# Kernel tuning notes

Measured on AMD Instinct MI355X. Metric: run time of the kernel, lower is better.

The kernel has to match this reference:

```python
import jax, jax.numpy as jnp
import numpy as np

H = 512          # hidden_dim
T = 80           # future_length
M = 6            # num_modes
OD = 2           # output_dim
B = 2048         # batch
TEMP = 1.2


def _lin_params(key, out_dim, in_dim, scale=0.02):
    kw, kb = jax.random.split(key)
    W = jax.random.normal(kw, (out_dim, in_dim), jnp.float32) * scale
    b = jax.random.normal(kb, (out_dim,), jnp.float32) * scale
    return W, b


def _per_mode(key, out_dim, in_dim, scale=0.02):
    ks = jax.random.split(key, M)
    Ws, bs = [], []
    for k in ks:
        W, b = _lin_params(k, out_dim, in_dim, scale)
        Ws.append(W); bs.append(b)
    return jnp.stack(Ws), jnp.stack(bs)


def setup_inputs() -> dict:
    key = jax.random.key(0)
    ks = jax.random.split(key, 20)
    inp = {}
    inp['composed_features'] = jax.random.normal(ks[0], (B, H), jnp.float32)
    # mode_decoders: Linear(H,2H) ReLU [Dropout] Linear(2H,H) ReLU [Dropout] Linear(H,H)
    inp['md_W1'], inp['md_b1'] = _per_mode(ks[1], 2 * H, H)
    inp['md_W2'], inp['md_b2'] = _per_mode(ks[2], H, 2 * H)
    inp['md_W3'], inp['md_b3'] = _per_mode(ks[3], H, H)
    # initial_hidden_projections: Linear(H, 2H)
    inp['ih_W'], inp['ih_b'] = _per_mode(ks[4], 2 * H, H)
    # time_projection (shared): Linear(1, H//2) ReLU Linear(H//2, H)
    inp['tp_W1'], inp['tp_b1'] = _lin_params(ks[5], H // 2, 1)
    inp['tp_W2'], inp['tp_b2'] = _lin_params(ks[6], H, H // 2)
    # feedback_projections: Linear(OD, H//2)
    inp['fb_W'], inp['fb_b'] = _per_mode(ks[7], H // 2, OD)
    # LSTM (2 layers, torch gate order i,f,g,o), per mode
    inp['l0_Wih'], inp['l0_bih'] = _per_mode(ks[8], 4 * H, H)
    inp['l0_Whh'], inp['l0_bhh'] = _per_mode(ks[9], 4 * H, H)
    inp['l1_Wih'], inp['l1_bih'] = _per_mode(ks[10], 4 * H, H)
    inp['l1_Whh'], inp['l1_bhh'] = _per_mode(ks[11], 4 * H, H)
    # output_projections: Linear(H,H) ReLU [Dropout] Linear(H,OD)
    inp['op_W1'], inp['op_b1'] = _per_mode(ks[12], H, H)
    inp['op_W2'], inp['op_b2'] = _per_mode(ks[13], OD, H)
    # confidence_head (shared): Linear(H, H//2) ReLU [Dropout] Linear(H//2, M)
    inp['cf_W1'], inp['cf_b1'] = _lin_params(ks[14], H // 2, H)
    inp['cf_W2'], inp['cf_b2'] = _lin_params(ks[15], M, H // 2)
    return inp


def _lstm_cell(x, h, c, Wih, Whh, bih, bhh):
    g = x @ Wih.T + h @ Whh.T + (bih + bhh)
    i, f, gg, o = jnp.split(g, 4, axis=-1)
    c_new = jax.nn.sigmoid(f) * c + jax.nn.sigmoid(i) * jnp.tanh(gg)
    h_new = jax.nn.sigmoid(o) * jnp.tanh(c_new)
    return h_new, c_new


def _forward(composed_features,
             md_W1, md_b1, md_W2, md_b2, md_W3, md_b3,
             ih_W, ih_b, tp_W1, tp_b1, tp_W2, tp_b2,
             fb_W, fb_b,
             l0_Wih, l0_bih, l0_Whh, l0_bhh,
             l1_Wih, l1_bih, l1_Whh, l1_bhh,
             op_W1, op_b1, op_W2, op_b2,
             cf_W1, cf_b1, cf_W2, cf_b2):
    x = composed_features
    bsz = x.shape[0]
    # shared time embeddings for all steps: [T, H]
    t_norm = (jnp.arange(T, dtype=jnp.float32) / (T - 1))[:, None]
    time_embs = jax.nn.relu(t_norm @ tp_W1.T + tp_b1) @ tp_W2.T + tp_b2

    def run_mode(mW1, mb1, mW2, mb2, mW3, mb3, iW, ib, fW, fb,
                 W0i, b0i, W0h, b0h, W1i, b1i, W1h, b1h,
                 oW1, ob1, oW2, ob2):
        # mode decoder (dropout = identity in eval)
        mf = jax.nn.relu(x @ mW1.T + mb1)
        mf = jax.nn.relu(mf @ mW2.T + mb2)
        mf = mf @ mW3.T + mb3                      # [B, H]
        init = x @ iW.T + ib                       # [B, 2H]
        h0 = init[:, :H]; c0 = init[:, H:]
        carry = (h0, c0, h0, c0, jnp.zeros((bsz, OD), x.dtype))
        pad = H - H // 2

        def step(carry, te_t):
            h0, c0, h1, c1, prev = carry
            fb_half = prev @ fW.T + fb             # [B, H//2]
            fb_full = jnp.pad(fb_half, ((0, 0), (0, pad)))
            xin = mf + 0.5 * te_t[None, :] + 0.3 * fb_full
            h0, c0 = _lstm_cell(xin, h0, c0, W0i, W0h, b0i, b0h)
            h1, c1 = _lstm_cell(h0, h1, c1, W1i, W1h, b1i, b1h)
            out = jax.nn.relu(h1 @ oW1.T + ob1) @ oW2.T + ob2  # [B, OD]
            return (h0, c0, h1, c1, out), out

        _, outs = jax.lax.scan(step, carry, time_embs)   # [T, B, OD]
        traj = jnp.transpose(outs, (1, 0, 2))            # [B, T, OD]
        return traj.at[:, 0, :].set(0.0)

    trajs = jax.vmap(run_mode)(md_W1, md_b1, md_W2, md_b2, md_W3, md_b3,
                               ih_W, ih_b, fb_W, fb_b,
                               l0_Wih, l0_bih, l0_Whh, l0_bhh,
                               l1_Wih, l1_bih, l1_Whh, l1_bhh,
                               op_W1, op_b1, op_W2, op_b2)  # [M, B, T, OD]
    trajectories = jnp.transpose(trajs, (1, 0, 2, 3))       # [B, M, T, OD]
    logits = jax.nn.relu(x @ cf_W1.T + cf_b1) @ cf_W2.T + cf_b2  # [B, M]
    confidences = jax.nn.softmax(logits / TEMP, axis=-1)
    return trajectories, confidences, logits


def reference(composed_features,
              md_W1, md_b1, md_W2, md_b2, md_W3, md_b3,
              ih_W, ih_b, tp_W1, tp_b1, tp_W2, tp_b2,
              fb_W, fb_b,
              l0_Wih, l0_bih, l0_Whh, l0_bhh,
              l1_Wih, l1_bih, l1_Whh, l1_bhh,
              op_W1, op_b1, op_W2, op_b2,
              cf_W1, cf_b1, cf_W2, cf_b2):
    return _forward(composed_features,
                    md_W1, md_b1, md_W2, md_b2, md_W3, md_b3,
                    ih_W, ih_b, tp_W1, tp_b1, tp_W2, tp_b2,
                    fb_W, fb_b,
                    l0_Wih, l0_bih, l0_Whh, l0_bhh,
                    l1_Wih, l1_bih, l1_Whh, l1_bhh,
                    op_W1, op_b1, op_W2, op_b2,
                    cf_W1, cf_b1, cf_W2, cf_b2)
```

## Files before the change

### kernel.cpp

```cpp
#include <hip/hip_runtime.h>
#include <cstdint>

typedef __bf16 bf16;
typedef __bf16 bf16x8 __attribute__((ext_vector_type(8)));
typedef float f32x4 __attribute__((ext_vector_type(4)));

#define DI __device__ __forceinline__

#define BATCH 2048
#define HD 512
#define NM 6

DI float sigmoidf_(float x){ return 1.0f / (1.0f + __expf(-x)); }
DI float tanhf_(float x){
  float a = __expf(-2.0f * fabsf(x));
  float t = (1.0f - a) / (1.0f + a);
  return __builtin_copysignf(t, x);
}

__global__ void k_diag(float* out, float wsmb){
  if (threadIdx.x == 0 && blockIdx.x == 0) out[0] = wsmb * 1.0e6f;
}

template<bool GATES, bool DUAL>
__global__ void k_pack(bf16* __restrict__ dst, const float* __restrict__ s1,
                       const float* __restrict__ s2, int K, int NROW, int ksplit)
{
  long idx = (long)blockIdx.x * 256 + threadIdx.x;
  int kper = K >> 3;
  int k0 = (int)(idx % kper) * 8;
  long rest = idx / kper;
  int p = (int)(rest % NROW);
  int mm = (int)(rest / NROW);
  int r;
  if (GATES){
    int nb2 = p >> 7, hi = (p >> 6) & 1, g = (p >> 4) & 3, jl = p & 15;
    r = g * 512 + nb2 * 32 + hi * 16 + jl;
  } else r = p;
  const float* src;
  if (DUAL){
    if (k0 >= ksplit) src = s2 + ((long)mm * NROW + r) * ksplit + (k0 - ksplit);
    else              src = s1 + ((long)mm * NROW + r) * ksplit + k0;
  } else {
    src = s1 + ((long)mm * NROW + r) * K + k0;
  }
  f32x4 v0 = *(const f32x4*)(src);
  f32x4 v1 = *(const f32x4*)(src + 4);
  bf16x8 o;
  #pragma unroll
  for (int k = 0; k < 4; ++k){ o[k] = (bf16)v0[k]; o[4+k] = (bf16)v1[k]; }
  *(bf16x8*)(dst + ((long)mm * NROW + p) * K + k0) = o;
}

__global__ void k_temb(bf16* tembb, const float* tpW1, const float* tpb1,
                       const float* tpW2, const float* tpb2)
{
  int t = blockIdx.x; int tid = threadIdx.x;
  __shared__ float rq[256];
  float tn = (t < 80) ? (float)t / 79.0f : 0.0f;
  rq[tid] = fmaxf(tn * tpW1[tid] + tpb1[tid], 0.0f);
  __syncthreads();
  for (int d = tid; d < 512; d += 256){
    float s = tpb2[d];
    const float* w = tpW2 + d * 256;
    for (int q = 0; q < 256; ++q) s += rq[q] * w[q];
    tembb[t * 512 + d] = (bf16)((t < 80) ? 0.5f * s : 0.0f);
  }
}

__global__ void k_biases(float* bias0p, float* bias1p,
                         const float* l0bih, const float* l0bhh,
                         const float* l1bih, const float* l1bhh,
                         const float* l0Wih, const float* fbb)
{
  int idx = blockIdx.x * 256 + threadIdx.x;
  int m = idx >> 11, p = idx & 2047;
  int nb2 = p >> 7, hi = (p >> 6) & 1, g = (p >> 4) & 3, jl = p & 15;
  int r = g * 512 + nb2 * 32 + hi * 16 + jl;
  bias1p[idx] = l1bih[m * 2048 + r] + l1bhh[m * 2048 + r];
  const float* wrow = l0Wih + ((long)m * 2048 + r) * 512;
  const float* fb = fbb + m * 256;
  float acc = 0.0f;
  for (int q = 0; q < 256; ++q) acc += fb[q] * wrow[q];
  bias0p[idx] = l0bih[m * 2048 + r] + l0bhh[m * 2048 + r] + 0.3f * acc;
}

__global__ void k_feffp(float* feffp, const float* fbW, const float* l0Wih)
{
  int idx = blockIdx.x * 256 + threadIdx.x;
  int p = idx & 2047, o = (idx >> 11) & 1, m = idx >> 12;
  int nb2 = p >> 7, hi = (p >> 6) & 1, g = (p >> 4) & 3, jl = p & 15;
  int r = g * 512 + nb2 * 32 + hi * 16 + jl;
  const float* wrow = l0Wih + ((long)m * 2048 + r) * 512;
  float acc = 0.0f;
  for (int q = 0; q < 256; ++q) acc += fbW[((long)m * 256 + q) * 2 + o] * wrow[q];
  feffp[((long)m * 2 + o) * 2048 + p] = 0.3f * acc;
}

__global__ void k_zero(float* part, float* traj)
{
  int i = blockIdx.x * 256 + threadIdx.x;
  part[i] = 0.0f;
  if (i < 24576){
    int od = i & 1, mm = (i >> 1) % 6, b = i / 12;
    traj[b * 960 + mm * 160 + od] = 0.0f;
  }
}

__global__ void k_logits(const bf16* lt1, const float* cfW2, const float* cfb2,
                         float* conf, float* logitsOut)
{
  int b = blockIdx.x * 256 + threadIdx.x;
  float acc[6];
  #pragma unroll
  for (int mm = 0; mm < 6; ++mm) acc[mm] = cfb2[mm];
  for (int q = 0; q < 256; ++q){
    float xv = (float)lt1[b * 256 + q];
    #pragma unroll
    for (int mm = 0; mm < 6; ++mm) acc[mm] += xv * cfW2[mm * 256 + q];
  }
  float mx = acc[0];
  #pragma unroll
  for (int mm = 1; mm < 6; ++mm) mx = fmaxf(mx, acc[mm]);
  float e[6], s = 0.0f;
  #pragma unroll
  for (int mm = 0; mm < 6; ++mm){ e[mm] = __expf((acc[mm] - mx) * (1.0f / 1.2f)); s += e[mm]; }
  float inv = 1.0f / s;
  #pragma unroll
  for (int mm = 0; mm < 6; ++mm){
    logitsOut[b * 6 + mm] = acc[mm];
    conf[b * 6 + mm] = e[mm] * inv;
  }
}

__global__ void k_red(const float* part, const float* opb2, float* traj)
{
  int i = blockIdx.x * 256 + threadIdx.x;
  int m = i >> 11, b = i & 2047;
  const float* pp = part + (long)i * 8;
  float o0 = pp[0] + pp[2] + pp[4] + pp[6] + opb2[m * 2];
  float o1 = pp[1] + pp[3] + pp[5] + pp[7] + opb2[m * 2 + 1];
  traj[(long)b * 960 + m * 160 + 158] = o0;
  traj[(long)b * 960 + m * 160 + 159] = o1;
}

struct GArgs {
  const bf16* A1; const bf16* A2; const bf16* Bw;
  long a1_ms, a2_ms, b_ms;
  int a_ld, K, ksplit, NBt, MBt, tprev;
  const float* biasf; long bias_ms;
  bf16* out_bf; long out_ms; int out_ld;
  float* out_f; long outf_ms;
  const bf16* baseb; long baseb_ms;
  const float* temb; long temb_ms;
  const float* feff; long feff_ms;
  const float* prevp;
  const float* ob2;
  const float* w2;
  float* part;
  float* cbuf; long c_ms;
  bf16* hout; long h_ms;
  bf16* hout2; float* cbuf2;
};

enum { EP_RELU = 0, EP_BF16 = 1, EP_F32 = 2, EP_INIT = 3, EP_LSTM = 4, EP_OUT = 5 };

template<int EP, bool SPLIT, bool FB>
__global__ __launch_bounds__(256, 2)
void gemm_k(GArgs a)
{
  __shared__ __attribute__((aligned(16))) char smem[33792];
  char* As = smem;
  char* Bs = smem + 16384;
  float* Gf = (float*)smem;

  const int id  = blockIdx.x;
  const int id2 = (id & 7) * ((int)gridDim.x >> 3) + (id >> 3);
  const int per = a.MBt * a.NBt;
  const int m   = id2 / per;
  const int rem = id2 - m * per;
  const int mb  = rem / a.NBt;
  const int nb  = rem - mb * a.NBt;

  const int tid = threadIdx.x;
  const int lane = tid & 63;
  const int wid  = tid >> 6;
  const int wr = wid >> 1, wc = wid & 1;

  const bf16* A1m = a.A1 + (long)m * a.a1_ms;
  const bf16* A2m = SPLIT ? (a.A2 + (long)m * a.a2_ms) : nullptr;
  const bf16* Bm  = a.Bw + (long)m * a.b_ms + (long)nb * 128 * a.K;

  f32x4 acc[4][4];
  #pragma unroll
  for (int i = 0; i < 4; ++i)
    #pragma unroll
    for (int j = 0; j < 4; ++j) acc[i][j] = f32x4{0.f, 0.f, 0.f, 0.f};

  f32x4 aR[4], bR[4];
  const int nk = a.K >> 6;

  auto loadT = [&](int kb){
    int kcol = kb << 6;
    const bf16* Asrc = A1m; int kl = kcol;
    if (SPLIT && kcol >= a.ksplit){ Asrc = A2m; kl = kcol - a.ksplit; }
    #pragma unroll
    for (int c = 0; c < 4; ++c){
      int off = c * 256 + tid;
      int r = off >> 3, s = off & 7;
      aR[c] = *(const f32x4*)(Asrc + (long)(mb * 128 + r) * a.a_ld + kl + s * 8);
      bR[c] = *(const f32x4*)(Bm + (long)r * a.K + kcol + s * 8);
    }
  };

  loadT(0);
  for (int kb = 0; kb < nk; ++kb){
    __syncthreads();
    #pragma unroll
    for (int c = 0; c < 4; ++c){
      int off = c * 256 + tid;
      int r = off >> 3, s = off & 7;
      int ph = (s * 16) ^ ((r & 7) << 4);
      *(f32x4*)(As + r * 128 + ph) = aR[c];
      *(f32x4*)(Bs + r * 128 + ph) = bR[c];
    }
    __syncthreads();
    if (kb + 1 < nk) loadT(kb + 1);
    #pragma unroll
    for (int ks = 0; ks < 2; ++ks){
      bf16x8 af[4], bg[4];
      #pragma unroll
      for (int f = 0; f < 4; ++f){
        int rr = wr * 64 + f * 16 + (lane & 15);
        int kB = ks * 64 + ((lane >> 4) << 4);
        af[f] = *(const bf16x8*)(As + rr * 128 + (kB ^ ((rr & 7) << 4)));
        int rb = wc * 64 + f * 16 + (lane & 15);
        bg[f] = *(const bf16x8*)(Bs + rb * 128 + (kB ^ ((rb & 7) << 4)));
      }
      #pragma unroll
      for (int i = 0; i < 4; ++i)
        #pragma unroll
        for (int j = 0; j < 4; ++j)
          acc[i][j] = __builtin_amdgcn_mfma_f32_16x16x32_bf16(af[i], bg[j], acc[i][j], 0, 0, 0);
    }
  }

  if constexpr (EP == EP_LSTM){
    const int jl = lane & 15;
    const int qr = lane >> 4;
    const int jh = nb * 32 + wc * 16 + jl;
    const long pbase = (long)nb * 128 + wc * 64 + jl;
    float addv[4], f0v[4], f1v[4];
    #pragma unroll
    for (int g = 0; g < 4; ++g){
      long p = pbase + g * 16;
      if constexpr (FB){
        addv[g] = a.temb[(long)m * a.temb_ms + p];
        f0v[g]  = a.feff[(long)m * a.feff_ms + p];
        f1v[g]  = a.feff[(long)m * a.feff_ms + 2048 + p];
      } else {
        addv[g] = a.biasf[(long)m * a.bias_ms + p];
      }
    }
    const bf16* bb = FB ? (a.baseb + (long)m * a.baseb_ms + pbase) : nullptr;
    float* cb = a.cbuf + (long)m * a.c_ms + jh;
    bf16*  hb = a.hout + (long)m * a.h_ms + jh;
    #pragma unroll
    for (int i = 0; i < 4; ++i){
      #pragma unroll
      for (int q = 0; q < 4; ++q){
        int b = mb * 128 + wr * 64 + i * 16 + qr * 4 + q;
        float pv0 = 0.f, pv1 = 0.f;
        if constexpr (FB){
          if (a.tprev >= 0){
            const float* pp = a.prevp + ((long)m * 2048 + b) * 8;
            pv0 = pp[0] + pp[2] + pp[4] + pp[6] + a.ob2[m * 2];
            pv1 = pp[1] + pp[3] + pp[5] + pp[7] + a.ob2[m * 2 + 1];
          }
          if (nb == 0 && wc == 0 && jl == 0 && a.tprev >= 1){
            a.out_f[(long)b * 960 + m * 160 + a.tprev * 2 + 0] = pv0;
            a.out_f[(long)b * 960 + m * 160 + a.tprev * 2 + 1] = pv1;
          }
        }
        float g4[4];
        #pragma unroll
        for (int g = 0; g < 4; ++g){
          float v = acc[i][g][q] + addv[g];
          if constexpr (FB){
            v += (float)bb[(long)b * 2048 + g * 16];
            v += pv0 * f0v[g] + pv1 * f1v[g];
          }
          g4[g] = v;
        }
        long ro = (long)b * HD;
        float ci = sigmoidf_(g4[0]), cf = sigmoidf_(g4[1]);
        float cg = tanhf_(g4[2]),    co = sigmoidf_(g4[3]);
        float cn = cf * cb[ro] + ci * cg;
        cb[ro] = cn;
        hb[ro] = (bf16)(co * tanhf_(cn));
      }
    }
    return;
  }

  if constexpr (EP == EP_OUT){
    __syncthreads();
    float* ps = (float*)smem;
    int colbase = wc * 64 + (lane & 15);
    float bv[4], w0v[4], w1v[4];
    #pragma unroll
    for (int j = 0; j < 4; ++j){
      int p = nb * 128 + colbase + j * 16;
      bv[j]  = a.biasf[(long)m * a.bias_ms + p];
      w0v[j] = a.w2[(long)m * 1024 + p];
      w1v[j] = a.w2[(long)m * 1024 + 512 + p];
    }
    #pragma unroll
    for (int i = 0; i < 4; ++i)
      #pragma unroll
      for (int q = 0; q < 4; ++q){
        float s0 = 0.f, s1 = 0.f;
        #pragma unroll
        for (int j = 0; j < 4; ++j){
          float v = fmaxf(acc[i][j][q] + bv[j], 0.0f);
          s0 += v * w0v[j]; s1 += v * w1v[j];
        }
        #pragma unroll
        for (int o2 = 1; o2 < 16; o2 <<= 1){ s0 += __shfl_xor(s0, o2); s1 += __shfl_xor(s1, o2); }
        if ((lane & 15) == 0){
          int row = wr * 64 + i * 16 + ((lane >> 4) << 2) + q;
          ps[row * 4 + wc * 2 + 0] = s0;
          ps[row * 4 + wc * 2 + 1] = s1;
        }
      }
    __syncthreads();
    if (tid < 128){
      int b = mb * 128 + tid;
      float o0 = ps[tid * 4 + 0] + ps[tid * 4 + 2];
      float o1 = ps[tid * 4 + 1] + ps[tid * 4 + 3];
      a.part[((long)m * 2048 + b) * 8 + nb * 2 + 0] = o0;
      a.part[((long)m * 2048 + b) * 8 + nb * 2 + 1] = o1;
    }
    return;
  }

  #pragma unroll 1
  for (int ph = 0; ph < 2; ++ph){
    __syncthreads();
    if (wc == ph){
      #pragma unroll
      for (int i = 0; i < 4; ++i)
        #pragma unroll
        for (int j = 0; j < 4; ++j)
          #pragma unroll
          for (int q = 0; q < 4; ++q){
            int rr = wr * 64 + i * 16 + ((lane >> 4) << 2) + q;
            int cc = j * 16 + (lane & 15);
            Gf[rr * 66 + cc] = acc[i][j][q];
          }
    }
    __syncthreads();

    #pragma unroll 1
    for (int it = 0; it < 4; ++it){
      int u = it * 256 + tid;
      int r = u >> 3, cg = u & 7;
      int b = mb * 128 + r;
      int p0 = nb * 128 + ph * 64 + cg * 8;
      float v[8];
      #pragma unroll
      for (int k2 = 0; k2 < 8; ++k2){
        v[k2] = Gf[r * 66 + cg * 8 + k2];
        if (a.biasf) v[k2] += a.biasf[(long)m * a.bias_ms + p0 + k2];
        if constexpr (EP == EP_RELU) v[k2] = fmaxf(v[k2], 0.0f);
      }
      if constexpr (EP == EP_F32){
        float* dst = a.out_f + (long)m * a.outf_ms + (long)b * a.out_ld + p0;
        #pragma unroll
        for (int k2 = 0; k2 < 8; ++k2) dst[k2] = v[k2];
      } else if constexpr (EP == EP_INIT){
        if (p0 < HD){
          bf16x8 ov;
          #pragma unroll
          for (int k2 = 0; k2 < 8; ++k2) ov[k2] = (bf16)v[k2];
          *(bf16x8*)(a.hout  + (long)m * a.h_ms + (long)b * HD + p0) = ov;
          *(bf16x8*)(a.hout2 + (long)m * a.h_ms + (long)b * HD + p0) = ov;
        } else {
          int p1 = p0 - HD;
          float* d1 = a.cbuf  + (long)m * a.c_ms + (long)b * HD + p1;
          float* d2 = a.cbuf2 + (long)m * a.c_ms + (long)b * HD + p1;
          #pragma unroll
          for (int k2 = 0; k2 < 8; ++k2){ d1[k2] = v[k2]; d2[k2] = v[k2]; }
        }
      } else {
        bf16x8 ov;
        #pragma unroll
        for (int k2 = 0; k2 < 8; ++k2) ov[k2] = (bf16)v[k2];
        *(bf16x8*)(a.out_bf + (long)m * a.out_ms + (long)b * a.out_ld + p0) = ov;
      }
    }
  }
}

extern "C" void kernel_launch(void* const* d_in, const int* in_sizes, int n_in,
                              void* d_out, int out_size, void* d_ws, size_t ws_size,
                              hipStream_t stream)
{
  (void)in_sizes; (void)n_in; (void)out_size;
  const float* X     = (const float*)d_in[0];
  const float* mdW1  = (const float*)d_in[1];
  const float* mdb1  = (const float*)d_in[2];
  const float* mdW2  = (const float*)d_in[3];
  const float* mdb2  = (const float*)d_in[4];
  const float* mdW3  = (const float*)d_in[5];
  const float* mdb3  = (const float*)d_in[6];
  const float* ihW   = (const float*)d_in[7];
  const float* ihb   = (const float*)d_in[8];
  const float* tpW1  = (const float*)d_in[9];
  const float* tpb1  = (const float*)d_in[10];
  const float* tpW2  = (const float*)d_in[11];
  const float* tpb2  = (const float*)d_in[12];
  const float* fbW   = (const float*)d_in[13];
  const float* fbb   = (const float*)d_in[14];
  const float* l0Wih = (const float*)d_in[15];
  const float* l0bih = (const float*)d_in[16];
  const float* l0Whh = (const float*)d_in[17];
  const float* l0bhh = (const float*)d_in[18];
  const float* l1Wih = (const float*)d_in[19];
  const float* l1bih = (const float*)d_in[20];
  const float* l1Whh = (const float*)d_in[21];
  const float* l1bhh = (const float*)d_in[22];
  const float* opW1  = (const float*)d_in[23];
  const float* opb1  = (const float*)d_in[24];
  const float* opW2  = (const float*)d_in[25];
  const float* opb2  = (const float*)d_in[26];
  const float* cfW1  = (const float*)d_in[27];
  const float* cfb1  = (const float*)d_in[28];
  const float* cfW2  = (const float*)d_in[29];
  const float* cfb2  = (const float*)d_in[30];
  float* out = (float*)d_out;

  const size_t NEED = 211009536;
  if (ws_size < NEED){
    k_diag<<<1, 64, 0, stream>>>(out, (float)(ws_size >> 20));
    return;
  }
  char* ws = (char*)d_ws;
  const long BH = (long)BATCH * HD;

  bf16*  Wp0     = (bf16*) (ws + 0);
  bf16*  Wp1     = (bf16*) (ws + 12582912);
  bf16*  WpO     = (bf16*) (ws + 37748736);
  bf16*  base0p  = (bf16*) (ws + 40894464);
  float* tembW0p = (float*)(ws + 91226112);
  float* bias1p  = (float*)(ws + 97517568);
  float* Feffp   = (float*)(ws + 97566720);
  char*  REG     =          ws + 97763328;
  bf16*  h0b     = (bf16*) (REG + 0);
  bf16*  h1b     = (bf16*) (REG + 25165824);
  float* c0      = (float*)(REG + 50331648);
  float* c1      = (float*)(REG + 75497472);
  char*  MREG    =          ws + 198426624;

  bf16*  W0ip    = (bf16*) (REG + 0);
  bf16*  mdW1p   = (bf16*) (REG + 12582912);
  bf16*  mdW2p   = (bf16*) (REG + 18874368);
  bf16*  mdW3p   = (bf16*) (REG + 25165824);
  bf16*  tembb   = (bf16*) (REG + 28311552);
  float* bias0p  = (float*)(REG + 28442624);
  bf16*  lt1     = (bf16*) (REG + 28491776);
  bf16*  t1buf   = (bf16*) (REG + 29540352);
  bf16*  t2buf   = (bf16*) (REG + 54706176);
  bf16*  mfbuf   = (bf16*) (REG + 67289088);
  bf16*  xb      = (bf16*) (MREG + 0);
  bf16*  ihWp    = (bf16*) (MREG + 2097152);
  bf16*  cfW1p   = (bf16*) (MREG + 8388608);
  float* part    = (float*)(MREG + 8650752);

  k_pack<false,false><<<dim3(512),  256, 0, stream>>>(xb,    X,     nullptr, 512,  2048, 512);
  k_pack<true ,false><<<dim3(3072), 256, 0, stream>>>(Wp0,   l0Whh, nullptr, 512,  2048, 512);
  k_pack<true ,false><<<dim3(3072), 256, 0, stream>>>(W0ip,  l0Wih, nullptr, 512,  2048, 512);
  k_pack<true ,true ><<<dim3(6144), 256, 0, stream>>>(Wp1,   l1Wih, l1Whh,   1024, 2048, 512);
  k_pack<false,false><<<dim3(768),  256, 0, stream>>>(WpO,   opW1,  nullptr, 512,  512,  512);
  k_pack<false,false><<<dim3(1536), 256, 0, stream>>>(mdW1p, mdW1,  nullptr, 512,  1024, 512);
  k_pack<false,false><<<dim3(1536), 256, 0, stream>>>(mdW2p, mdW2,  nullptr, 1024, 512,  1024);
  k_pack<false,false><<<dim3(768),  256, 0, stream>>>(mdW3p, mdW3,  nullptr, 512,  512,  512);
  k_pack<false,false><<<dim3(1536), 256, 0, stream>>>(ihWp,  ihW,   nullptr, 512,  1024, 512);
  k_pack<false,false><<<dim3(64),   256, 0, stream>>>(cfW1p, cfW1,  nullptr, 512,  256,  512);

  k_temb  <<<dim3(128), 256, 0, stream>>>(tembb, tpW1, tpb1, tpW2, tpb2);
  k_biases<<<dim3(48),  256, 0, stream>>>(bias0p, bias1p, l0bih, l0bhh, l1bih, l1bhh, l0Wih, fbb);
  k_feffp <<<dim3(96),  256, 0, stream>>>(Feffp, fbW, l0Wih);
  k_zero  <<<dim3(384), 256, 0, stream>>>(part, out);

  { GArgs g{}; g.A1 = xb; g.a1_ms = 0; g.a_ld = 512; g.Bw = mdW1p; g.b_ms = (long)1024*512;
    g.K = 512; g.ksplit = 512; g.NBt = 8; g.MBt = 16; g.biasf = mdb1; g.bias_ms = 1024;
    g.out_bf = t1buf; g.out_ms = (long)2048*1024; g.out_ld = 1024;
    gemm_k<EP_RELU,false,false><<<dim3(16*8*6), 256, 0, stream>>>(g); }
  { GArgs g{}; g.A1 = t1buf; g.a1_ms = (long)2048*1024; g.a_ld = 1024; g.Bw = mdW2p; g.b_ms = (long)512*1024;
    g.K = 1024; g.ksplit = 1024; g.NBt = 4; g.MBt = 16; g.biasf = mdb2; g.bias_ms = 512;
    g.out_bf = t2buf; g.out_ms = BH; g.out_ld = 512;
    gemm_k<EP_RELU,false,false><<<dim3(16*4*6), 256, 0, stream>>>(g); }
  { GArgs g{}; g.A1 = t2buf; g.a1_ms = BH; g.a_ld = 512; g.Bw = mdW3p; g.b_ms = (long)512*512;
    g.K = 512; g.ksplit = 512; g.NBt = 4; g.MBt = 16; g.biasf = mdb3; g.bias_ms = 512;
    g.out_bf = mfbuf; g.out_ms = BH; g.out_ld = 512;
    gemm_k<EP_BF16,false,false><<<dim3(16*4*6), 256, 0, stream>>>(g); }
  { GArgs g{}; g.A1 = tembb; g.a1_ms = 0; g.a_ld = 512; g.Bw = W0ip; g.b_ms = (long)2048*512;
    g.K = 512; g.ksplit = 512; g.NBt = 16; g.MBt = 1; g.biasf = nullptr;
    g.out_f = tembW0p; g.outf_ms = (long)128*2048; g.out_ld = 2048;
    gemm_k<EP_F32,false,false><<<dim3(1*16*6), 256, 0, stream>>>(g); }
  { GArgs g{}; g.A1 = mfbuf; g.a1_ms = BH; g.a_ld = 512; g.Bw = W0ip; g.b_ms = (long)2048*512;
    g.K = 512; g.ksplit = 512; g.NBt = 16; g.MBt = 16; g.biasf = bias0p; g.bias_ms = 2048;
    g.out_bf = base0p; g.out_ms = (long)2048*2048; g.out_ld = 2048;
    gemm_k<EP_BF16,false,false><<<dim3(16*16*6), 256, 0, stream>>>(g); }
  { GArgs g{}; g.A1 = xb; g.a1_ms = 0; g.a_ld = 512; g.Bw = cfW1p; g.b_ms = 0;
    g.K = 512; g.ksplit = 512; g.NBt = 2; g.MBt = 16; g.biasf = cfb1; g.bias_ms = 0;
    g.out_bf = lt1; g.out_ms = 0; g.out_ld = 256;
    gemm_k<EP_RELU,false,false><<<dim3(16*2*1), 256, 0, stream>>>(g); }
  k_logits<<<dim3(8), 256, 0, stream>>>(lt1, cfW2, cfb2, out + 1966080, out + 1966080 + 12288);
  { GArgs g{}; g.A1 = xb; g.a1_ms = 0; g.a_ld = 512; g.Bw = ihWp; g.b_ms = (long)1024*512;
    g.K = 512; g.ksplit = 512; g.NBt = 8; g.MBt = 16; g.biasf = ihb; g.bias_ms = 1024;
    g.hout = h0b; g.h_ms = BH; g.hout2 = h1b; g.cbuf = c0; g.c_ms = BH; g.cbuf2 = c1;
    gemm_k<EP_INIT,false,false><<<dim3(16*8*6), 256, 0, stream>>>(g); }

  for (int t = 0; t < 80; ++t){
    int cur = t & 1, nxt = cur ^ 1;
    { GArgs g{}; g.A1 = h0b + (size_t)cur * 6 * BH; g.a1_ms = BH; g.a_ld = 512;
      g.Bw = Wp0; g.b_ms = (long)2048*512; g.K = 512; g.ksplit = 512; g.NBt = 16; g.MBt = 16;
      g.tprev = t - 1;
      g.baseb = base0p; g.baseb_ms = (long)2048*2048;
      g.temb = tembW0p + (long)t * 2048; g.temb_ms = (long)128*2048;
      g.feff = Feffp; g.feff_ms = 4096;
      g.prevp = part; g.ob2 = opb2; g.out_f = out;
      g.cbuf = c0; g.c_ms = BH;
      g.hout = h0b + (size_t)nxt * 6 * BH; g.h_ms = BH;
      gemm_k<EP_LSTM,false,true><<<dim3(16*16*6), 256, 0, stream>>>(g); }
    { GArgs g{}; g.A1 = h0b + (size_t)nxt * 6 * BH; g.A2 = h1b + (size_t)cur * 6 * BH;
      g.a1_ms = BH; g.a2_ms = BH; g.a_ld = 512;
      g.Bw = Wp1; g.b_ms = (long)2048*1024; g.K = 1024; g.ksplit = 512; g.NBt = 16; g.MBt = 16;
      g.biasf = bias1p; g.bias_ms = 2048;
      g.cbuf = c1; g.c_ms = BH;
      g.hout = h1b + (size_t)nxt * 6 * BH; g.h_ms = BH;
      gemm_k<EP_LSTM,true,false><<<dim3(16*16*6), 256, 0, stream>>>(g); }
    { GArgs g{}; g.A1 = h1b + (size_t)nxt * 6 * BH; g.a1_ms = BH; g.a_ld = 512;
      g.Bw = WpO; g.b_ms = (long)512*512; g.K = 512; g.ksplit = 512; g.NBt = 4; g.MBt = 16;
      g.biasf = opb1; g.bias_ms = 512;
      g.w2 = opW2; g.part = part;
      gemm_k<EP_OUT,false,false><<<dim3(16*4*6), 256, 0, stream>>>(g); }
  }
  k_red<<<dim3(48), 256, 0, stream>>>(part, opb2, out);
}
```

Before: 11.57 ms.

## Stage GEMM tiles via direct global-to-LDS loads and prefetch after fragment reads

Replaces the register-staged global loads and LDS stores in the GEMM main loop with global_load_lds direct copies, keeping the XOR swizzle through per-lane source offsets. Each iteration now reads all LDS fragments into registers first, syncs, then issues the next tile's async loads before running the MFMAs. This removes the VGPR round trip and one explicit LDS write phase per k-block. It raises fragment register pressure and depends on implicit completion of the LDS DMA at the barrier.

```diff
diff --git a/kernel.cpp b/kernel.cpp
--- a/kernel.cpp
+++ b/kernel.cpp
@@ -16,6 +16,12 @@
   float a = __expf(-2.0f * fabsf(x));
   float t = (1.0f - a) / (1.0f + a);
   return __builtin_copysignf(t, x);
+}
+
+DI void gload16(const bf16* g, char* l){
+  __builtin_amdgcn_global_load_lds(
+    (const __attribute__((address_space(1))) void*)g,
+    (__attribute__((address_space(3))) void*)l, 16, 0, 0);
 }
 
 __global__ void k_diag(float* out, float wsmb){
@@ -197,52 +203,56 @@
     #pragma unroll
     for (int j = 0; j < 4; ++j) acc[i][j] = f32x4{0.f, 0.f, 0.f, 0.f};
 
-  f32x4 aR[4], bR[4];
+  const int rl = lane >> 3;
+  const int sg = (lane & 7) ^ rl;
+  const bf16* a1B[4]; const bf16* a2B[4]; const bf16* bB[4];
+  char* ldA[4]; char* ldB[4];
+  #pragma unroll
+  for (int c = 0; c < 4; ++c){
+    int rt = (wid * 4 + c) * 8 + rl;
+    a1B[c] = A1m + (long)(mb * 128 + rt) * a.a_ld + sg * 8;
+    if (SPLIT) a2B[c] = A2m + (long)(mb * 128 + rt) * a.a_ld + sg * 8;
+    bB[c]  = Bm + (long)rt * a.K + sg * 8;
+    ldA[c] = As + (wid * 4 + c) * 1024;
+    ldB[c] = Bs + (wid * 4 + c) * 1024;
+  }
+  auto STAGE = [&](int kb){
+    int kcol = kb << 6;
+    if (SPLIT && kcol >= a.ksplit){
+      int kl = kcol - a.ksplit;
+      #pragma unroll
+      for (int c = 0; c < 4; ++c){ gload16(a2B[c] + kl, ldA[c]); gload16(bB[c] + kcol, ldB[c]); }
+    } else {
+      #pragma unroll
+      for (int c = 0; c < 4; ++c){ gload16(a1B[c] + kcol, ldA[c]); gload16(bB[c] + kcol, ldB[c]); }
+    }
+  };
+
   const int nk = a.K >> 6;
-
-  auto loadT = [&](int kb){
-    int kcol = kb << 6;
-    const bf16* Asrc = A1m; int kl = kcol;
-    if (SPLIT && kcol >= a.ksplit){ Asrc = A2m; kl = kcol - a.ksplit; }
-    #pragma unroll
-    for (int c = 0; c < 4; ++c){
-      int off = c * 256 + tid;
-      int r = off >> 3, s = off & 7;
-      aR[c] = *(const f32x4*)(Asrc + (long)(mb * 128 + r) * a.a_ld + kl + s * 8);
-      bR[c] = *(const f32x4*)(Bm + (long)r * a.K + kcol + s * 8);
-    }
-  };
-
-  loadT(0);
+  STAGE(0);
   for (int kb = 0; kb < nk; ++kb){
     __syncthreads();
-    #pragma unroll
-    for (int c = 0; c < 4; ++c){
-      int off = c * 256 + tid;
-      int r = off >> 3, s = off & 7;
-      int ph = (s * 16) ^ ((r & 7) << 4);
-      *(f32x4*)(As + r * 128 + ph) = aR[c];
-      *(f32x4*)(Bs + r * 128 + ph) = bR[c];
-    }
-    __syncthreads();
-    if (kb + 1 < nk) loadT(kb + 1);
+    bf16x8 af[2][4], bg[2][4];
     #pragma unroll
     for (int ks = 0; ks < 2; ++ks){
-      bf16x8 af[4], bg[4];
       #pragma unroll
       for (int f = 0; f < 4; ++f){
         int rr = wr * 64 + f * 16 + (lane & 15);
         int kB = ks * 64 + ((lane >> 4) << 4);
-        af[f] = *(const bf16x8*)(As + rr * 128 + (kB ^ ((rr & 7) << 4)));
+        af[ks][f] = *(const bf16x8*)(As + rr * 128 + (kB ^ ((rr & 7) << 4)));
         int rb = wc * 64 + f * 16 + (lane & 15);
-        bg[f] = *(const bf16x8*)(Bs + rb * 128 + (kB ^ ((rb & 7) << 4)));
+        bg[ks][f] = *(const bf16x8*)(Bs + rb * 128 + (kB ^ ((rb & 7) << 4)));
       }
+    }
+    __syncthreads();
+    if (kb + 1 < nk) STAGE(kb + 1);
+    #pragma unroll
+    for (int ks = 0; ks < 2; ++ks)
       #pragma unroll
       for (int i = 0; i < 4; ++i)
         #pragma unroll
         for (int j = 0; j < 4; ++j)
-          acc[i][j] = __builtin_amdgcn_mfma_f32_16x16x32_bf16(af[i], bg[j], acc[i][j], 0, 0, 0);
-    }
+          acc[i][j] = __builtin_amdgcn_mfma_f32_16x16x32_bf16(af[ks][i], bg[ks][j], acc[i][j], 0, 0, 0);
   }
 
   if constexpr (EP == EP_LSTM){
```

Result: faster. 11.30 ms, median of 2 (-2.4%).
